# Kernel optimization log

Measured on AMD Instinct MI355X. Metric: run time of the kernel, lower is better.

## Reference

```python
import jax, jax.numpy as jnp
import numpy as np

OBS_LEN, PRED_LEN, N, P = 8, 12, 4096, 32
EH, DH, EMB, BOT, NZ = 64, 128, 64, 1024, 8


def setup_inputs() -> dict:
    key = jax.random.key(0)
    ks = iter(jax.random.split(key, 64))
    rn = lambda shp, s=0.05: (jax.random.normal(next(ks), shp, jnp.float32) * s)
    d = {
        'obs_traj': rn((OBS_LEN, N, 2), 1.0),
        'obs_traj_rel': rn((OBS_LEN, N, 2), 0.5),
        'obs_speed': jax.random.uniform(next(ks), (OBS_LEN, N, 1), jnp.float32),
        'noise': rn((N, NZ), 1.0),
        'enc_emb_W': rn((2, EMB)), 'enc_emb_b': jnp.zeros((EMB,), jnp.float32),
        'enc_Wih': rn((EMB, 4 * EH)), 'enc_Whh': rn((EH, 4 * EH)), 'enc_b': jnp.zeros((4 * EH,), jnp.float32),
        'pool_sp_W': rn((2, 64)), 'pool_sp_b': jnp.zeros((64,), jnp.float32),
        'pool_spd_W': rn((1, 64)), 'pool_spd_b': jnp.zeros((64,), jnp.float32),
        'pool_l1_W': rn((192, 512)), 'pool_l1_b': jnp.zeros((512,), jnp.float32),
        'pool_bn1_g': jnp.ones((512,), jnp.float32), 'pool_bn1_b': jnp.zeros((512,), jnp.float32),
        'pool_l2_W': rn((512, BOT)), 'pool_l2_b': jnp.zeros((BOT,), jnp.float32),
        'pool_bn2_g': jnp.ones((BOT,), jnp.float32), 'pool_bn2_b': jnp.zeros((BOT,), jnp.float32),
        'spd_emb_W': rn((OBS_LEN, 64)), 'spd_emb_b': jnp.zeros((64,), jnp.float32),
        'ctx_l1_W': rn((EH + BOT + 64, 1024)), 'ctx_l1_b': jnp.zeros((1024,), jnp.float32),
        'ctx_bn1_g': jnp.ones((1024,), jnp.float32), 'ctx_bn1_b': jnp.zeros((1024,), jnp.float32),
        'ctx_l2_W': rn((1024, DH - NZ)), 'ctx_l2_b': jnp.zeros((DH - NZ,), jnp.float32),
        'ctx_bn2_g': jnp.ones((DH - NZ,), jnp.float32), 'ctx_bn2_b': jnp.zeros((DH - NZ,), jnp.float32),
        'dec_emb_W': rn((3, EMB)), 'dec_emb_b': jnp.zeros((EMB,), jnp.float32),
        'dec_Wih': rn((EMB, 4 * DH)), 'dec_Whh': rn((DH, 4 * DH)), 'dec_b': jnp.zeros((4 * DH,), jnp.float32),
        'h2p_W': rn((DH, 2)), 'h2p_b': jnp.zeros((2,), jnp.float32),
        'group_size': P,
    }
    return d


def _lstm(xs, Wih, Whh, b, h0, c0):
    # xs: [T, B, in]; PyTorch gate order (i, f, g, o)
    def step(carry, x):
        h, c = carry
        g = x @ Wih + h @ Whh + b
        i, f, gg, o = jnp.split(g, 4, axis=-1)
        c = jax.nn.sigmoid(f) * c + jax.nn.sigmoid(i) * jnp.tanh(gg)
        h = jax.nn.sigmoid(o) * jnp.tanh(c)
        return (h, c), h
    (h, c), _ = jax.lax.scan(step, (h0, c0), xs)
    return h, c


def _bn(x, g, b):
    # BatchNorm1d, eval mode with running_mean=0, running_var=1
    return x * g + b


def reference(obs_traj, obs_traj_rel, obs_speed, noise,
              enc_emb_W, enc_emb_b, enc_Wih, enc_Whh, enc_b,
              pool_sp_W, pool_sp_b, pool_spd_W, pool_spd_b,
              pool_l1_W, pool_l1_b, pool_bn1_g, pool_bn1_b,
              pool_l2_W, pool_l2_b, pool_bn2_g, pool_bn2_b,
              spd_emb_W, spd_emb_b,
              ctx_l1_W, ctx_l1_b, ctx_bn1_g, ctx_bn1_b,
              ctx_l2_W, ctx_l2_b, ctx_bn2_g, ctx_bn2_b,
              dec_emb_W, dec_emb_b, dec_Wih, dec_Whh, dec_b,
              h2p_W, h2p_b, group_size):
    n = obs_traj.shape[1]
    G = n // group_size
    # ---- Encoder: embed rel traj, run LSTM, take final hidden ----
    emb = obs_traj_rel @ enc_emb_W + enc_emb_b                       # [T, N, 64]
    h0 = jnp.zeros((n, EH), emb.dtype)
    final_h, _ = _lstm(emb, enc_Wih, enc_Whh, enc_b, h0, h0)         # [N, 64]
    # ---- PoolHiddenNet (vectorized per-group P x P social pooling) ----
    end_pos = obs_traj[-1].reshape(G, group_size, 2)                 # [G, P, 2]
    end_spd = obs_speed[-1].reshape(G, group_size, 1)                # [G, P, 1]
    hG = final_h.reshape(G, group_size, EH)                          # [G, P, 64]
    # rel[g, i, j] = pos[g, j] - pos[g, i]
    rel = end_pos[:, None, :, :] - end_pos[:, :, None, :]            # [G, P, P, 2]
    rel_e = rel @ pool_sp_W + pool_sp_b                              # [G, P, P, 64]
    spd_e = end_spd @ pool_spd_W + pool_spd_b                        # [G, P, 64]
    Pn = group_size
    feat = jnp.concatenate([
        rel_e,
        jnp.broadcast_to(hG[:, None, :, :], (G, Pn, Pn, EH)),
        jnp.broadcast_to(spd_e[:, None, :, :], (G, Pn, Pn, 64)),
    ], axis=-1)                                                      # [G, P, P, 192]
    h1 = jax.nn.relu(_bn(feat @ pool_l1_W + pool_l1_b, pool_bn1_g, pool_bn1_b))
    h2 = jax.nn.relu(_bn(h1 @ pool_l2_W + pool_l2_b, pool_bn2_g, pool_bn2_b))
    pool_h = jnp.max(h2, axis=2).reshape(n, BOT)                     # max over j -> [N, 1024]
    # ---- speed context: sigmoid(Linear(8 -> 64)) over obs speed history ----
    spd_hist = jnp.transpose(obs_speed[:, :, 0])                     # [N, 8]
    speed_ctx = jax.nn.sigmoid(spd_hist @ spd_emb_W + spd_emb_b)     # [N, 64]
    # ---- mlp_decoder_context + ped-level noise ----
    ctx_in = jnp.concatenate([final_h, pool_h, speed_ctx], axis=1)   # [N, 1152]
    c1 = jax.nn.relu(_bn(ctx_in @ ctx_l1_W + ctx_l1_b, ctx_bn1_g, ctx_bn1_b))
    ctx = jax.nn.relu(_bn(c1 @ ctx_l2_W + ctx_l2_b, ctx_bn2_g, ctx_bn2_b))  # [N, 120]
    dec_h = jnp.concatenate([ctx, noise], axis=1)                    # [N, 128]
    dec_c = jnp.zeros_like(dec_h)
    # ---- Decoder rollout (pred_len steps) ----
    last_pos = obs_traj[-1]
    last_speed = obs_speed[-1]                                       # [N, 1]
    x0 = jnp.concatenate([obs_traj_rel[-1], last_speed], axis=1) @ dec_emb_W + dec_emb_b

    def step(carry, _):
        h, c, x, lp = carry
        g = x @ dec_Wih + h @ dec_Whh + dec_b
        i, f, gg, o = jnp.split(g, 4, axis=-1)
        c = jax.nn.sigmoid(f) * c + jax.nn.sigmoid(i) * jnp.tanh(gg)
        h = jax.nn.sigmoid(o) * jnp.tanh(c)
        rel_pos = h @ h2p_W + h2p_b                                  # [N, 2]
        cur = rel_pos + lp
        x = jnp.concatenate([rel_pos, last_speed], axis=1) @ dec_emb_W + dec_emb_b
        return (h, c, x, cur), rel_pos

    _, rels = jax.lax.scan(step, (dec_h, dec_c, x0, last_pos), None, length=PRED_LEN)
    return rels  # [pred_len, N, 2]
```

## Files before the change

### kernel.cpp

```cpp
#include <hip/hip_runtime.h>

typedef __attribute__((ext_vector_type(8))) short v8s;
typedef __attribute__((ext_vector_type(4))) float v4f;
typedef unsigned short u16;

#define DINL static __device__ __forceinline__

DINL float b2f(u16 u){ union { unsigned uu; float ff; } x; x.uu = ((unsigned)u)<<16; return x.ff; }
DINL u16 f2b(float f){ union { float ff; unsigned uu; } x; x.ff = f; unsigned r = x.uu + 0x7FFFu + ((x.uu>>16)&1u); return (u16)(r>>16); }
DINL u16 f2b_hu(float f){ union { float ff; unsigned uu; } x; x.ff = f; return (u16)((x.uu + 0x8000u)>>16); }
DINL float sigm(float x){ return 1.0f/(1.0f+__expf(-x)); }
DINL float tanh_(float x){ return 2.0f/(1.0f+__expf(-2.0f*x)) - 1.0f; }
DINL float ld(const void* p, int i, int isf){
    return isf ? ((const float*)p)[i] : b2f(((const u16*)p)[i]);
}
DINL void g2lds16(const u16* g, u16* l){
    __builtin_amdgcn_global_load_lds(
        (const __attribute__((address_space(1))) unsigned int*)g,
        (__attribute__((address_space(3))) unsigned int*)l, 16, 0, 0);
}
DINL int detect_isf(const void* obs_speed){
    const u16* p = (const u16*)obs_speed;
    int f = 0;
    for (int i = 0; i < 16; ++i){
        u16 v = p[2*i];
        if ((v & 0x8000u) || v > 0x3F80u) f = 1;
    }
    return f;
}

#define FLAG_OFF 0x000000
#define AUX_OFF  0x000100
#define ENCF_OFF 0x010000
#define DECF_OFF 0x020000
#define CW2T_OFF 0x050000
#define W2T_OFF  0x090000
#define DECH_OFF 0x090000
#define CW1T_OFF 0x190000
#define IT_OFF   0x3D0000
#define IR_OFF   0x3F0000
#define IS_OFF   0x410000
#define INZ_OFF  0x420000
#define IW1H_OFF 0x430000
#define SM_OFF   0x440000
#define CTX_OFF  0x450000
#define AV_OFF   0xD50000
#define BIG_NEED 0x1550000

#define SM_EEW 0
#define SM_EEB 128
#define SM_ENB 192
#define SM_DEW 448
#define SM_DEB 640
#define SM_DNB 704
#define SM_H2W 1216
#define SM_H2B 1472
#define SM_SEW 1536
#define SM_SEB 2048

DINL void trans_tile(const void* in, u16* out, int K, int N, int isf,
                     int bx, int by, int t, float tile[64][65])
{
    const int nbase = bx*64, kbase = by*64;
    const int c = t & 63, r0 = (t >> 6)*16;
    for (int rep = 0; rep < 16; ++rep){
        int r = r0 + rep;
        int n = nbase + c;
        float v = 0.f;
        if (n < N) v = ld(in, (kbase + r)*N + n, isf);
        tile[r][c] = v;
    }
    __syncthreads();
    for (int rep = 0; rep < 16; ++rep){
        int r = r0 + rep;
        out[(size_t)(nbase + r)*K + kbase + c] = f2b(tile[c][r]);
    }
}

__global__ __launch_bounds__(256) void k_prep(
    const void* obs_traj, const void* obs_rel, const void* obs_speed, const void* noise,
    const void* eeW, const void* eeB, const void* enc_Wih, const void* enc_Whh, const void* encB,
    const void* spW, const void* spB, const void* spdW, const void* spdB,
    const void* pool_l1_W, const void* l1B, const void* bn1g, const void* bn1b,
    const void* pool_l2_W, const void* l2b, const void* bn2g, const void* bn2b,
    const void* seW, const void* seB,
    const void* ctx_l1_W, const void* c1b, const void* cbn1g, const void* cbn1b,
    const void* ctx_l2_W, const void* c2b, const void* cbn2g, const void* cbn2b,
    const void* deW, const void* deB, const void* dec_Wih, const void* dec_Whh, const void* decB,
    const void* h2W, const void* h2B,
    int* flag, float* AUX,
    u16* IT, u16* IR, u16* IS, u16* INZ, u16* IW1H, u16* SM,
    u16* W2T, u16* cW1T, u16* cW2T, u16* encF, u16* decF)
{
    __shared__ float tile[64][65];
    __shared__ int sisf;
    const int t = threadIdx.x;
    if (t == 0){
        int f = detect_isf(obs_speed);
        sisf = f;
        if (blockIdx.x == 0) *flag = f;
    }
    __syncthreads();
    const int isf = sisf;
    int bid = blockIdx.x;
    if (bid < 905){
        int idx = bid*256 + t;
        if (idx < 65536){ IT[idx] = f2b(ld(obs_traj, idx, isf)); return; }
        idx -= 65536;
        if (idx < 65536){ IR[idx] = f2b(ld(obs_rel, idx, isf)); return; }
        idx -= 65536;
        if (idx < 32768){ IS[idx] = f2b(ld(obs_speed, idx, isf)); return; }
        idx -= 32768;
        if (idx < 32768){ INZ[idx] = f2b(ld(noise, idx, isf)); return; }
        idx -= 32768;
        if (idx < 32768){ IW1H[idx] = f2b(ld(pool_l1_W, idx + 32768, isf)); return; }
        idx -= 32768;
        if (idx < 128){ SM[SM_EEW + idx] = f2b(ld(eeW, idx, isf)); return; }
        idx -= 128;
        if (idx < 64){ SM[SM_EEB + idx] = f2b(ld(eeB, idx, isf)); return; }
        idx -= 64;
        if (idx < 256){ SM[SM_ENB + idx] = f2b(ld(encB, idx, isf)); return; }
        idx -= 256;
        if (idx < 192){ SM[SM_DEW + idx] = f2b(ld(deW, idx, isf)); return; }
        idx -= 192;
        if (idx < 64){ SM[SM_DEB + idx] = f2b(ld(deB, idx, isf)); return; }
        idx -= 64;
        if (idx < 512){ SM[SM_DNB + idx] = f2b(ld(decB, idx, isf)); return; }
        idx -= 512;
        if (idx < 256){ SM[SM_H2W + idx] = f2b(ld(h2W, idx, isf)); return; }
        idx -= 256;
        if (idx < 2){ SM[SM_H2B + idx] = f2b(ld(h2B, idx, isf)); return; }
        idx -= 2;
        if (idx < 512){ SM[SM_SEW + idx] = f2b(ld(seW, idx, isf)); return; }
        idx -= 512;
        if (idx < 64){ SM[SM_SEB + idx] = f2b(ld(seB, idx, isf)); return; }
        return;
    }
    bid -= 905;
    if (bid < 512){
        int idx = bid*256 + t;
        if (idx < 32768){
            int jj = idx&7, lane = (idx>>3)&63, kcnf = idx>>9;
            int kc = kcnf&3, nf = kcnf>>2;
            int k = kc*32 + (lane>>4)*8 + jj, n = nf*16 + (lane&15);
            encF[idx] = (k < 64) ? f2b(ld(enc_Wih, k*256+n, isf)) : f2b(ld(enc_Whh, (k-64)*256+n, isf));
        } else {
            idx -= 32768;
            int jj = idx&7, lane = (idx>>3)&63, kcnf = idx>>9;
            int kc = kcnf % 6, nf = kcnf / 6;
            int k = kc*32 + (lane>>4)*8 + jj, n = nf*16 + (lane&15);
            decF[idx] = (k < 64) ? f2b(ld(dec_Wih, k*512+n, isf)) : f2b(ld(dec_Whh, (k-64)*512+n, isf));
        }
        return;
    }
    bid -= 512;
    if (bid < 128){ trans_tile(pool_l2_W, W2T, 512, 1024, isf, bid & 15, bid >> 4, t, tile); return; }
    bid -= 128;
    if (bid < 288){ trans_tile(ctx_l1_W, cW1T, 1152, 1024, isf, bid & 15, bid >> 4, t, tile); return; }
    bid -= 288;
    if (bid < 32){ trans_tile(ctx_l2_W, cW2T, 1024, 120, isf, bid & 1, bid >> 1, t, tile); return; }
    bid -= 32;
    {
        int idx = bid*256 + t;
        if (idx < 512){
            int c = idx;
            float m0 = 0.f, m1 = 0.f, qv = 0.f, cv = 0.f;
            for (int e = 0; e < 64; ++e){
                float w1a = ld(pool_l1_W, e*512 + c, isf);
                m0 += ld(spW, e, isf)*w1a;
                m1 += ld(spW, 64+e, isf)*w1a;
                cv += ld(spB, e, isf)*w1a;
                float w1c = ld(pool_l1_W, (128+e)*512 + c, isf);
                qv += ld(spdW, e, isf)*w1c;
                cv += ld(spdB, e, isf)*w1c;
            }
            cv += ld(l1B, c, isf);
            float g1 = ld(bn1g, c, isf), bb1 = ld(bn1b, c, isf);
            AUX[c] = m0; AUX[512+c] = m1; AUX[1024+c] = qv; AUX[1536+c] = cv;
            AUX[2048+c] = g1; AUX[2560+c] = bb1;
            AUX[3072+c] = g1*m0; AUX[3584+c] = g1*m1;
            return;
        }
        idx -= 512;
        if (idx < 1024){
            float g = ld(bn2g, idx, isf);
            AUX[4096+idx] = g; AUX[5120+idx] = ld(l2b, idx, isf)*g + ld(bn2b, idx, isf);
            return;
        }
        idx -= 1024;
        if (idx < 1024){
            float g = ld(cbn1g, idx, isf);
            AUX[6144+idx] = g; AUX[7168+idx] = ld(c1b, idx, isf)*g + ld(cbn1b, idx, isf);
            return;
        }
        idx -= 1024;
        if (idx < 128){
            int c = idx;
            float g  = (c < 120) ? ld(cbn2g, c, isf) : 1.f;
            float bb = (c < 120) ? (ld(c2b, c, isf)*g + ld(cbn2b, c, isf)) : 0.f;
            AUX[8192+c] = g; AUX[8320+c] = bb;
        }
    }
}

__global__ __launch_bounds__(256) void k_encoder(
    const u16* __restrict__ rel, const u16* __restrict__ embW, const u16* __restrict__ embB,
    const u16* __restrict__ encF, const u16* __restrict__ encB,
    const u16* __restrict__ IT, const u16* __restrict__ IS, const u16* __restrict__ IW1H,
    const u16* __restrict__ sW, const u16* __restrict__ sB,
    const float* __restrict__ AUX,
    u16* __restrict__ ctxIn, u16* __restrict__ Avec)
{
    __shared__ __align__(16) u16 Als[16*136];
    __shared__ float pxs[16], pys[16], sps[16];
    const int t = threadIdx.x, pedbase = blockIdx.x*16;
    const int w = t>>6, lane = t&63, quad = lane>>4, l15 = lane&15;
    for (int idx = t; idx < 16*64; idx += 256){ int p = idx>>6, jj = idx&63; Als[p*136 + 64 + jj] = 0; }
    if (t < 16){
        pxs[t] = b2f(IT[7*8192 + (pedbase+t)*2 + 0]);
        pys[t] = b2f(IT[7*8192 + (pedbase+t)*2 + 1]);
        sps[t] = b2f(IS[7*4096 + pedbase + t]);
    }
    {
        int p = t>>4, e0 = (t&15)*4;
        float rx = b2f(rel[(pedbase+p)*2 + 0]);
        float ry = b2f(rel[(pedbase+p)*2 + 1]);
        for (int e = e0; e < e0+4; ++e)
            Als[p*136 + e] = f2b(rx*b2f(embW[e]) + ry*b2f(embW[64+e]) + b2f(embB[e]));
    }
    const int j = w*16 + l15;
    const float bi = b2f(encB[j]), bff = b2f(encB[64+j]), bg = b2f(encB[128+j]), bo = b2f(encB[192+j]);
    float c4[4] = {0.f,0.f,0.f,0.f};
    for (int step = 0; step < 8; ++step){
        __syncthreads();
        v4f acc[4];
        for (int q = 0; q < 4; ++q) acc[q] = (v4f){0.f,0.f,0.f,0.f};
        for (int kc = 0; kc < 4; ++kc){
            v8s a = *(const v8s*)&Als[l15*136 + kc*32 + quad*8];
            for (int q = 0; q < 4; ++q){
                int nf = q*4 + w;
                v8s b = *(const v8s*)&encF[((nf*4 + kc)*64 + lane)*8];
                acc[q] = __builtin_amdgcn_mfma_f32_16x16x32_bf16(a, b, acc[q], 0, 0, 0);
            }
        }
        __syncthreads();
        for (int r = 0; r < 4; ++r){
            float gi = sigm(acc[0][r] + bi), gf = sigm(acc[1][r] + bff);
            float gg = tanh_(acc[2][r] + bg), go = sigm(acc[3][r] + bo);
            c4[r] = gf*c4[r] + gi*gg;
            Als[(quad*4 + r)*136 + 64 + j] = f2b(go*tanh_(c4[r]));
        }
        if (step < 7){
            int p = t>>4, e0 = (t&15)*4;
            float rx = b2f(rel[(step+1)*8192 + (pedbase+p)*2 + 0]);
            float ry = b2f(rel[(step+1)*8192 + (pedbase+p)*2 + 1]);
            for (int e = e0; e < e0+4; ++e)
                Als[p*136 + e] = f2b(rx*b2f(embW[e]) + ry*b2f(embW[64+e]) + b2f(embB[e]));
        }
    }
    __syncthreads();
    for (int idx = t; idx < 1024; idx += 256){
        int p = idx>>6, e = idx&63;
        ctxIn[(size_t)(pedbase+p)*1152 + e] = Als[p*136 + 64 + e];
    }
    {
        const int c0 = (t&127)*4, pg = (t>>7)*8;
        float4 acc[8];
        for (int p = 0; p < 8; ++p) acc[p] = make_float4(0.f,0.f,0.f,0.f);
        for (int e = 0; e < 64; ++e){
            ushort4 wv = *(const ushort4*)(IW1H + e*512 + c0);
            float w0 = b2f(wv.x), w1 = b2f(wv.y), w2 = b2f(wv.z), w3 = b2f(wv.w);
            for (int p = 0; p < 8; ++p){
                float h = b2f(Als[(pg+p)*136 + 64 + e]);
                acc[p].x += h*w0; acc[p].y += h*w1; acc[p].z += h*w2; acc[p].w += h*w3;
            }
        }
        float4 m0 = *(const float4*)(AUX + c0),        m1 = *(const float4*)(AUX + 512 + c0);
        float4 qv = *(const float4*)(AUX + 1024 + c0), cv = *(const float4*)(AUX + 1536 + c0);
        float4 g1 = *(const float4*)(AUX + 2048 + c0), bb = *(const float4*)(AUX + 2560 + c0);
        for (int p = 0; p < 8; ++p){
            float px = pxs[pg+p], py = pys[pg+p], sp = sps[pg+p];
            ushort4 o;
            o.x = f2b(g1.x*(px*m0.x + py*m1.x + sp*qv.x + cv.x + acc[p].x) + bb.x);
            o.y = f2b(g1.y*(px*m0.y + py*m1.y + sp*qv.y + cv.y + acc[p].y) + bb.y);
            o.z = f2b(g1.z*(px*m0.z + py*m1.z + sp*qv.z + cv.z + acc[p].z) + bb.z);
            o.w = f2b(g1.w*(px*m0.w + py*m1.w + sp*qv.w + cv.w + acc[p].w) + bb.w);
            *(ushort4*)&Avec[(size_t)(pedbase+pg+p)*512 + c0] = o;
        }
    }
    {
        int s = t & 63;
        for (int rep = 0; rep < 4; ++rep){
            int p = (t>>6)*4 + rep;
            int nid = pedbase + p;
            float a = b2f(sB[s]);
            for (int tt = 0; tt < 8; ++tt) a += b2f(IS[tt*4096 + nid]) * b2f(sW[tt*64 + s]);
            ctxIn[(size_t)nid*1152 + 1088 + s] = f2b(sigm(a));
        }
    }
}

__global__ __launch_bounds__(256, 3) void k_pool(
    const u16* __restrict__ Avec, const u16* __restrict__ W2T,
    const u16* __restrict__ IT, const float* __restrict__ AUX,
    u16* __restrict__ ctxIn)
{
    __shared__ __align__(16) u16 Als[64*72];
    __shared__ __align__(16) u16 Bls[256*64];
    __shared__ float auxM[1024];
    __shared__ float pxs[2], pys[2];
    const int t = threadIdx.x;
    const int g = blockIdx.x >> 4, ip = blockIdx.x & 15;
    const int n0 = blockIdx.y * 256;
    const int w = t>>6, lane = t&63, quad = lane>>4, l15 = lane&15;
    const int aj = t>>3, ao = t&7;
    for (int i = t; i < 1024; i += 256) auxM[i] = AUX[3072 + i];
    if (t < 2){
        pxs[t] = b2f(IT[7*8192 + (g*32 + ip*2 + t)*2 + 0]);
        pys[t] = b2f(IT[7*8192 + (g*32 + ip*2 + t)*2 + 1]);
    }
    const u16* bsrc = W2T + (size_t)(n0 + w*8 + (lane>>3))*512 + (size_t)(((lane&7) ^ (lane>>3)))*8;
    u16* bdst = &Bls[w*512];
    const u16* arow = Avec + (size_t)(g*32+aj)*512 + ao*8;
    v4f acc[4][4];
    for (int mf = 0; mf < 4; ++mf) for (int nf = 0; nf < 4; ++nf) acc[mf][nf] = (v4f){0.f,0.f,0.f,0.f};
    union { v8s v; u16 u[8]; } av;
    av.v = *(const v8s*)arow;
    for (int ch = 0; ch < 8; ++ch){
        const int k0 = ch*64;
        __syncthreads();
        for (int it = 0; it < 8; ++it)
            g2lds16(bsrc + k0 + it*16384, bdst + it*2048);
        {
            float a0[8], m0a[8], m1a[8];
            for (int i = 0; i < 8; ++i) a0[i] = b2f(av.u[i]);
            *(float4*)(m0a)   = *(const float4*)&auxM[k0 + ao*8];
            *(float4*)(m0a+4) = *(const float4*)&auxM[k0 + ao*8 + 4];
            *(float4*)(m1a)   = *(const float4*)&auxM[512 + k0 + ao*8];
            *(float4*)(m1a+4) = *(const float4*)&auxM[512 + k0 + ao*8 + 4];
            for (int il = 0; il < 2; ++il){
                float npx = -pxs[il], npy = -pys[il];
                union { v8s v; u16 u[8]; } pk;
                for (int i = 0; i < 8; ++i){
                    float v = __builtin_fmaf(npy, m1a[i], __builtin_fmaf(npx, m0a[i], a0[i]));
                    pk.u[i] = f2b_hu(fmaxf(v, 0.f));
                }
                *(v8s*)&Als[(il*32+aj)*72 + ao*8] = pk.v;
            }
        }
        if (ch < 7) av.v = *(const v8s*)(arow + (ch+1)*64);
        __syncthreads();
        for (int kc = 0; kc < 2; ++kc){
            v8s af[4];
            for (int mf = 0; mf < 4; ++mf)
                af[mf] = *(const v8s*)&Als[(mf*16 + l15)*72 + kc*32 + quad*8];
            const int sl = ((kc*4 + quad) ^ (l15&7))*8;
            #pragma unroll
            for (int nf = 0; nf < 4; ++nf){
                v8s bf = *(const v8s*)&Bls[(w*64 + nf*16 + l15)*64 + sl];
                acc[0][nf] = __builtin_amdgcn_mfma_f32_16x16x32_bf16(af[0], bf, acc[0][nf], 0, 0, 0);
                acc[1][nf] = __builtin_amdgcn_mfma_f32_16x16x32_bf16(af[1], bf, acc[1][nf], 0, 0, 0);
                acc[2][nf] = __builtin_amdgcn_mfma_f32_16x16x32_bf16(af[2], bf, acc[2][nf], 0, 0, 0);
                acc[3][nf] = __builtin_amdgcn_mfma_f32_16x16x32_bf16(af[3], bf, acc[3][nf], 0, 0, 0);
            }
        }
    }
    const float* S2 = AUX + 4096; const float* B2 = AUX + 5120;
    for (int nf = 0; nf < 4; ++nf){
        int n = n0 + w*64 + nf*16 + l15;
        float s = S2[n], bb = B2[n];
        float mm0 = 0.f, mm1 = 0.f;
        for (int mf = 0; mf < 2; ++mf) for (int r = 0; r < 4; ++r) mm0 = fmaxf(mm0, fmaxf(s*acc[mf][nf][r] + bb, 0.f));
        for (int mf = 2; mf < 4; ++mf) for (int r = 0; r < 4; ++r) mm1 = fmaxf(mm1, fmaxf(s*acc[mf][nf][r] + bb, 0.f));
        mm0 = fmaxf(mm0, __shfl_xor(mm0, 16)); mm0 = fmaxf(mm0, __shfl_xor(mm0, 32));
        mm1 = fmaxf(mm1, __shfl_xor(mm1, 16)); mm1 = fmaxf(mm1, __shfl_xor(mm1, 32));
        if (quad == 0) ctxIn[(size_t)(g*32 + ip*2 + 0)*1152 + 64 + n] = f2b(mm0);
        if (quad == 1) ctxIn[(size_t)(g*32 + ip*2 + 1)*1152 + 64 + n] = f2b(mm1);
    }
}

template<int MF>
__global__ __launch_bounds__(256) void k_gemm_bt(
    const u16* __restrict__ A, int lda, const u16* __restrict__ BT,
    const float* __restrict__ S, const float* __restrict__ Bb,
    u16* __restrict__ out, int ldo, int K, int validN,
    const u16* __restrict__ noisep)
{
    __shared__ __align__(16) u16 Als[MF*32*72];
    __shared__ __align__(16) u16 Bls[128*72];
    const int t = threadIdx.x;
    const int m0 = blockIdx.x*(MF*32), n0 = blockIdx.y*128;
    const int w = t>>6, lane = t&63, quad = lane>>4, l15 = lane&15;
    const int rw = w>>1, cw = w&1;
    v4f acc[MF][4];
    for (int mf = 0; mf < MF; ++mf) for (int nf = 0; nf < 4; ++nf) acc[mf][nf] = (v4f){0.f,0.f,0.f,0.f};
    const int nch = K >> 6;
    for (int ch = 0; ch < nch; ++ch){
        const int k0 = ch*64;
        __syncthreads();
        if (MF == 4){
            const int srow = t>>1, sh = t&1;
            const u16* srcA = A + (size_t)(m0+srow)*lda + k0 + sh*32;
            u16* dstA = &Als[srow*72 + sh*32];
            ((v8s*)dstA)[0] = ((const v8s*)srcA)[0];
            ((v8s*)dstA)[1] = ((const v8s*)srcA)[1];
            ((v8s*)dstA)[2] = ((const v8s*)srcA)[2];
            ((v8s*)dstA)[3] = ((const v8s*)srcA)[3];
        } else {
            const int srow = t>>2, sh = t&3;
            const u16* srcA = A + (size_t)(m0+srow)*lda + k0 + sh*16;
            u16* dstA = &Als[srow*72 + sh*16];
            ((v8s*)dstA)[0] = ((const v8s*)srcA)[0];
            ((v8s*)dstA)[1] = ((const v8s*)srcA)[1];
        }
        {
            const int srow = t>>1, sh = t&1;
            const u16* srcB = BT + (size_t)(n0+srow)*K + k0 + sh*32;
            u16* dstB = &Bls[srow*72 + sh*32];
            ((v8s*)dstB)[0] = ((const v8s*)srcB)[0];
            ((v8s*)dstB)[1] = ((const v8s*)srcB)[1];
            ((v8s*)dstB)[2] = ((const v8s*)srcB)[2];
            ((v8s*)dstB)[3] = ((const v8s*)srcB)[3];
        }
        __syncthreads();
        for (int kc = 0; kc < 2; ++kc){
            v8s af[MF], bf[4];
            for (int mf = 0; mf < MF; ++mf) af[mf] = *(const v8s*)&Als[(rw*(MF*16) + mf*16 + l15)*72 + kc*32 + quad*8];
            for (int nf = 0; nf < 4; ++nf) bf[nf] = *(const v8s*)&Bls[(cw*64 + nf*16 + l15)*72 + kc*32 + quad*8];
            for (int mf = 0; mf < MF; ++mf)
                for (int nf = 0; nf < 4; ++nf)
                    acc[mf][nf] = __builtin_amdgcn_mfma_f32_16x16x32_bf16(af[mf], bf[nf], acc[mf][nf], 0, 0, 0);
        }
    }
    for (int nf = 0; nf < 4; ++nf){
        int n = n0 + cw*64 + nf*16 + l15;
        bool okn = (n < validN);
        float s = okn ? S[n] : 0.f, bb = okn ? Bb[n] : 0.f;
        bool okz = (!okn) && (noisep != nullptr) && (n < 128);
        for (int mf = 0; mf < MF; ++mf){
            int m = m0 + rw*(MF*16) + mf*16 + quad*4;
            for (int r = 0; r < 4; ++r){
                float v = fmaxf(s*acc[mf][nf][r] + bb, 0.f);
                if (okn) out[(size_t)(m+r)*ldo + n] = f2b(v);
                else if (okz) out[(size_t)(m+r)*ldo + n] = noisep[(size_t)(m+r)*8 + (n - 120)];
            }
        }
    }
}

__global__ __launch_bounds__(256) void k_decoder(
    const u16* __restrict__ decH0, const u16* __restrict__ decF, const u16* __restrict__ decB,
    const u16* __restrict__ dembW, const u16* __restrict__ dembB,
    const u16* __restrict__ h2pW, const u16* __restrict__ h2pB,
    const u16* __restrict__ obs_rel, const u16* __restrict__ obs_speed,
    const int* __restrict__ flag, void* __restrict__ outp)
{
    __shared__ __align__(16) u16 Als[16*200];
    __shared__ float rps[16][2];
    __shared__ float sps[16];
    __shared__ float h2ps[256];
    const int t = threadIdx.x, pedbase = blockIdx.x*16;
    const int w = t>>6, lane = t&63, quad = lane>>4, l15 = lane&15;
    const int isf = *flag;
    for (int idx = t; idx < 2048; idx += 256){
        int p = idx>>7, jj = idx&127;
        Als[p*200 + 64 + jj] = decH0[(pedbase+p)*128 + jj];
    }
    h2ps[t] = b2f(h2pW[t]);
    if (t < 16) sps[t] = b2f(obs_speed[7*4096 + pedbase + t]);
    if (t < 32){ int p = t>>1, cmp = t&1; rps[p][cmp] = b2f(obs_rel[7*8192 + (pedbase+p)*2 + cmp]); }
    __syncthreads();
    {
        int p = t>>4, e0 = (t&15)*4;
        for (int e = e0; e < e0+4; ++e){
            float v = rps[p][0]*b2f(dembW[e]) + rps[p][1]*b2f(dembW[64+e]) + sps[p]*b2f(dembW[128+e]) + b2f(dembB[e]);
            Als[p*200 + e] = f2b(v);
        }
    }
    float bI[2], bF[2], bG[2], bO[2];
    for (int nfl = 0; nfl < 2; ++nfl){
        int j = w*32 + nfl*16 + l15;
        bI[nfl] = b2f(decB[j]); bF[nfl] = b2f(decB[128+j]);
        bG[nfl] = b2f(decB[256+j]); bO[nfl] = b2f(decB[384+j]);
    }
    float c8[2][4] = {{0.f,0.f,0.f,0.f},{0.f,0.f,0.f,0.f}};
    for (int s = 0; s < 12; ++s){
        __syncthreads();
        v4f acc[4][2];
        for (int q = 0; q < 4; ++q) for (int nfl = 0; nfl < 2; ++nfl) acc[q][nfl] = (v4f){0.f,0.f,0.f,0.f};
        for (int kc = 0; kc < 6; ++kc){
            v8s a = *(const v8s*)&Als[l15*200 + kc*32 + quad*8];
            for (int q = 0; q < 4; ++q){
                for (int nfl = 0; nfl < 2; ++nfl){
                    int nf = q*8 + w*2 + nfl;
                    v8s b = *(const v8s*)&decF[((nf*6 + kc)*64 + lane)*8];
                    acc[q][nfl] = __builtin_amdgcn_mfma_f32_16x16x32_bf16(a, b, acc[q][nfl], 0, 0, 0);
                }
            }
        }
        __syncthreads();
        for (int nfl = 0; nfl < 2; ++nfl){
            int j = w*32 + nfl*16 + l15;
            for (int r = 0; r < 4; ++r){
                float gi = sigm(acc[0][nfl][r] + bI[nfl]), gf = sigm(acc[1][nfl][r] + bF[nfl]);
                float gg = tanh_(acc[2][nfl][r] + bG[nfl]), go = sigm(acc[3][nfl][r] + bO[nfl]);
                c8[nfl][r] = gf*c8[nfl][r] + gi*gg;
                Als[(quad*4 + r)*200 + 64 + j] = f2b(go*tanh_(c8[nfl][r]));
            }
        }
        __syncthreads();
        {
            int p = t>>4, cmp = (t>>3)&1, part = t&7;
            float rp = 0.f;
            int j0 = part*16;
            for (int jj = j0; jj < j0+16; ++jj)
                rp += b2f(Als[p*200 + 64 + jj]) * h2ps[jj*2 + cmp];
            rp += __shfl_xor(rp, 1);
            rp += __shfl_xor(rp, 2);
            rp += __shfl_xor(rp, 4);
            if (part == 0){
                rp += b2f(h2pB[cmp]);
                int oi = s*8192 + (pedbase+p)*2 + cmp;
                if (isf) ((float*)outp)[oi] = rp;
                else     ((u16*)outp)[oi]   = f2b(rp);
                rps[p][cmp] = rp;
            }
        }
        __syncthreads();
        {
            int p = t>>4, e0 = (t&15)*4;
            for (int e = e0; e < e0+4; ++e){
                float v = rps[p][0]*b2f(dembW[e]) + rps[p][1]*b2f(dembW[64+e]) + sps[p]*b2f(dembW[128+e]) + b2f(dembB[e]);
                Als[p*200 + e] = f2b(v);
            }
        }
    }
}

extern "C" void kernel_launch(void* const* d_in, const int* in_sizes, int n_in,
                              void* d_out, int out_size, void* d_ws, size_t ws_size,
                              hipStream_t stream)
{
    (void)in_sizes; (void)n_in; (void)out_size;
    const void* obs_traj  = d_in[0];
    const void* obs_rel   = d_in[1];
    const void* obs_speed = d_in[2];
    const void* noise     = d_in[3];
    const void* enc_emb_W = d_in[4];
    const void* enc_emb_b = d_in[5];
    const void* enc_Wih   = d_in[6];
    const void* enc_Whh   = d_in[7];
    const void* enc_b     = d_in[8];
    const void* pool_sp_W = d_in[9];
    const void* pool_sp_b = d_in[10];
    const void* pool_spd_W= d_in[11];
    const void* pool_spd_b= d_in[12];
    const void* pool_l1_W = d_in[13];
    const void* pool_l1_b = d_in[14];
    const void* pool_bn1_g= d_in[15];
    const void* pool_bn1_b= d_in[16];
    const void* pool_l2_W = d_in[17];
    const void* pool_l2_b = d_in[18];
    const void* pool_bn2_g= d_in[19];
    const void* pool_bn2_b= d_in[20];
    const void* spd_emb_W = d_in[21];
    const void* spd_emb_b = d_in[22];
    const void* ctx_l1_W  = d_in[23];
    const void* ctx_l1_b  = d_in[24];
    const void* ctx_bn1_g = d_in[25];
    const void* ctx_bn1_b = d_in[26];
    const void* ctx_l2_W  = d_in[27];
    const void* ctx_l2_b  = d_in[28];
    const void* ctx_bn2_g = d_in[29];
    const void* ctx_bn2_b = d_in[30];
    const void* dec_emb_W = d_in[31];
    const void* dec_emb_b = d_in[32];
    const void* dec_Wih   = d_in[33];
    const void* dec_Whh   = d_in[34];
    const void* dec_b     = d_in[35];
    const void* h2p_W     = d_in[36];
    const void* h2p_b     = d_in[37];

    char* ws = (char*)d_ws;
    int*   flag  = (int*)  (ws + FLAG_OFF);
    float* AUX   = (float*)(ws + AUX_OFF);
    u16*   encF  = (u16*)  (ws + ENCF_OFF);
    u16*   decF  = (u16*)  (ws + DECF_OFF);
    u16*   cW2T  = (u16*)  (ws + CW2T_OFF);
    u16*   W2T   = (u16*)  (ws + W2T_OFF);
    u16*   decH  = (u16*)  (ws + DECH_OFF);
    u16*   cW1T  = (u16*)  (ws + CW1T_OFF);
    u16*   IT    = (u16*)  (ws + IT_OFF);
    u16*   IR    = (u16*)  (ws + IR_OFF);
    u16*   IS    = (u16*)  (ws + IS_OFF);
    u16*   INZ   = (u16*)  (ws + INZ_OFF);
    u16*   IW1H  = (u16*)  (ws + IW1H_OFF);
    u16*   SM    = (u16*)  (ws + SM_OFF);
    u16*   ctxIn = (u16*)  (ws + CTX_OFF);
    u16*   Avec  = (u16*)  (ws + AV_OFF);
    u16*   c1    = (u16*)  (ws + AV_OFF);
    const bool big = (ws_size >= (size_t)BIG_NEED);

    k_prep<<<dim3(1876), dim3(256), 0, stream>>>(
        obs_traj, obs_rel, obs_speed, noise,
        enc_emb_W, enc_emb_b, enc_Wih, enc_Whh, enc_b,
        pool_sp_W, pool_sp_b, pool_spd_W, pool_spd_b,
        pool_l1_W, pool_l1_b, pool_bn1_g, pool_bn1_b,
        pool_l2_W, pool_l2_b, pool_bn2_g, pool_bn2_b,
        spd_emb_W, spd_emb_b,
        ctx_l1_W, ctx_l1_b, ctx_bn1_g, ctx_bn1_b,
        ctx_l2_W, ctx_l2_b, ctx_bn2_g, ctx_bn2_b,
        dec_emb_W, dec_emb_b, dec_Wih, dec_Whh, dec_b,
        h2p_W, h2p_b,
        flag, AUX, IT, IR, IS, INZ, IW1H, SM,
        W2T, cW1T, cW2T, encF, decF);
    k_encoder<<<dim3(256), dim3(256), 0, stream>>>(
        IR, SM + SM_EEW, SM + SM_EEB, encF, SM + SM_ENB,
        IT, IS, IW1H, SM + SM_SEW, SM + SM_SEB, AUX, ctxIn, Avec);
    k_pool<<<dim3(2048, 4), dim3(256), 0, stream>>>(Avec, W2T, IT, AUX, ctxIn);
    if (big){
        k_gemm_bt<4><<<dim3(32, 8), dim3(256), 0, stream>>>(
            ctxIn, 1152, cW1T, AUX + 6144, AUX + 7168, c1, 1024, 1152, 1024, (const u16*)nullptr);
        k_gemm_bt<2><<<dim3(64, 1), dim3(256), 0, stream>>>(
            c1, 1024, cW2T, AUX + 8192, AUX + 8320, decH, 128, 1024, 120, INZ);
    } else {
        k_gemm_bt<4><<<dim3(16, 8), dim3(256), 0, stream>>>(
            ctxIn, 1152, cW1T, AUX + 6144, AUX + 7168, c1, 1024, 1152, 1024, (const u16*)nullptr);
        k_gemm_bt<2><<<dim3(32, 1), dim3(256), 0, stream>>>(
            c1, 1024, cW2T, AUX + 8192, AUX + 8320, decH, 128, 1024, 120, INZ);
        k_gemm_bt<4><<<dim3(16, 8), dim3(256), 0, stream>>>(
            ctxIn + (size_t)2048*1152, 1152, cW1T, AUX + 6144, AUX + 7168, c1, 1024, 1152, 1024, (const u16*)nullptr);
        k_gemm_bt<2><<<dim3(32, 1), dim3(256), 0, stream>>>(
            c1, 1024, cW2T, AUX + 8192, AUX + 8320, decH + (size_t)2048*128, 128, 1024, 120, INZ + (size_t)2048*8);
    }
    k_decoder<<<dim3(256), dim3(256), 0, stream>>>(
        decH, decF, SM + SM_DNB, SM + SM_DEW, SM + SM_DEB,
        SM + SM_H2W, SM + SM_H2B, IR, IS, flag, d_out);
}
```

Baseline: 439.2 us.

## Build the pool hidden layer once per block and loop over all output tiles

The pooling kernel now computes the full 64x512 first-layer activation (relative-position term plus ReLU) once into LDS with an XOR swizzle. It then loops over eight 128-column tiles of the second-layer weights inside a single block, instead of launching four y-blocks that each recompute the activation. This removes redundant activation recomputation and Avec reads, and cuts the grid from 8192 to 2048 blocks. In exchange LDS use grows to about 80KB per block, occupancy is lowered to 2 blocks, and each block runs a longer serial loop with two barriers per chunk.

Result: slower. 454.5 us (+3.5%).

```diff
diff --git a/kernel.cpp b/kernel.cpp
--- a/kernel.cpp
+++ b/kernel.cpp
@@ -300,82 +300,96 @@
     }
 }
 
-__global__ __launch_bounds__(256, 3) void k_pool(
+__global__ __launch_bounds__(256, 2) void k_pool(
     const u16* __restrict__ Avec, const u16* __restrict__ W2T,
     const u16* __restrict__ IT, const float* __restrict__ AUX,
     u16* __restrict__ ctxIn)
 {
-    __shared__ __align__(16) u16 Als[64*72];
-    __shared__ __align__(16) u16 Bls[256*64];
-    __shared__ float auxM[1024];
-    __shared__ float pxs[2], pys[2];
+    __shared__ __align__(16) u16 H1[64*512];
+    __shared__ __align__(16) u16 Bls[128*64];
     const int t = threadIdx.x;
     const int g = blockIdx.x >> 4, ip = blockIdx.x & 15;
-    const int n0 = blockIdx.y * 256;
     const int w = t>>6, lane = t&63, quad = lane>>4, l15 = lane&15;
     const int aj = t>>3, ao = t&7;
-    for (int i = t; i < 1024; i += 256) auxM[i] = AUX[3072 + i];
-    if (t < 2){
-        pxs[t] = b2f(IT[7*8192 + (g*32 + ip*2 + t)*2 + 0]);
-        pys[t] = b2f(IT[7*8192 + (g*32 + ip*2 + t)*2 + 1]);
-    }
-    const u16* bsrc = W2T + (size_t)(n0 + w*8 + (lane>>3))*512 + (size_t)(((lane&7) ^ (lane>>3)))*8;
+    const float px0 = b2f(IT[7*8192 + (g*32 + ip*2 + 0)*2 + 0]);
+    const float py0 = b2f(IT[7*8192 + (g*32 + ip*2 + 0)*2 + 1]);
+    const float px1 = b2f(IT[7*8192 + (g*32 + ip*2 + 1)*2 + 0]);
+    const float py1 = b2f(IT[7*8192 + (g*32 + ip*2 + 1)*2 + 1]);
+    const float* M0G = AUX + 3072;
+    const float* M1G = AUX + 3584;
+    const u16* arow = Avec + (size_t)(g*32 + aj)*512 + ao*8;
+    #pragma unroll
+    for (int ch = 0; ch < 8; ++ch){
+        union { v8s v; u16 u[8]; } av;
+        av.v = *(const v8s*)(arow + ch*64);
+        float a0[8], m0a[8], m1a[8];
+        *(float4*)(m0a)   = *(const float4*)&M0G[ch*64 + ao*8];
+        *(float4*)(m0a+4) = *(const float4*)&M0G[ch*64 + ao*8 + 4];
+        *(float4*)(m1a)   = *(const float4*)&M1G[ch*64 + ao*8];
+        *(float4*)(m1a+4) = *(const float4*)&M1G[ch*64 + ao*8 + 4];
+        for (int i = 0; i < 8; ++i) a0[i] = b2f(av.u[i]);
+        #pragma unroll
+        for (int il = 0; il < 2; ++il){
+            const float npx = (il == 0) ? -px0 : -px1;
+            const float npy = (il == 0) ? -py0 : -py1;
+            int r = il*32 + aj;
+            int slot = (ch*8 + ao) ^ (r & 7);
+            union { v8s v; u16 u[8]; } pk;
+            for (int i = 0; i < 8; ++i){
+                float v = __builtin_fmaf(npy, m1a[i], __builtin_fmaf(npx, m0a[i], a0[i]));
+                pk.u[i] = f2b_hu(fmaxf(v, 0.f));
+            }
+            *(v8s*)&H1[r*512 + slot*8] = pk.v;
+        }
+    }
+    const u16* bsrc = W2T + (size_t)(w*8 + (lane>>3))*512 + (size_t)((lane&7) ^ (lane>>3))*8;
     u16* bdst = &Bls[w*512];
-    const u16* arow = Avec + (size_t)(g*32+aj)*512 + ao*8;
-    v4f acc[4][4];
-    for (int mf = 0; mf < 4; ++mf) for (int nf = 0; nf < 4; ++nf) acc[mf][nf] = (v4f){0.f,0.f,0.f,0.f};
-    union { v8s v; u16 u[8]; } av;
-    av.v = *(const v8s*)arow;
-    for (int ch = 0; ch < 8; ++ch){
-        const int k0 = ch*64;
-        __syncthreads();
-        for (int it = 0; it < 8; ++it)
-            g2lds16(bsrc + k0 + it*16384, bdst + it*2048);
-        {
-            float a0[8], m0a[8], m1a[8];
-            for (int i = 0; i < 8; ++i) a0[i] = b2f(av.u[i]);
-            *(float4*)(m0a)   = *(const float4*)&auxM[k0 + ao*8];
-            *(float4*)(m0a+4) = *(const float4*)&auxM[k0 + ao*8 + 4];
-            *(float4*)(m1a)   = *(const float4*)&auxM[512 + k0 + ao*8];
-            *(float4*)(m1a+4) = *(const float4*)&auxM[512 + k0 + ao*8 + 4];
-            for (int il = 0; il < 2; ++il){
-                float npx = -pxs[il], npy = -pys[il];
-                union { v8s v; u16 u[8]; } pk;
-                for (int i = 0; i < 8; ++i){
-                    float v = __builtin_fmaf(npy, m1a[i], __builtin_fmaf(npx, m0a[i], a0[i]));
-                    pk.u[i] = f2b_hu(fmaxf(v, 0.f));
+    const float* S2 = AUX + 4096;
+    const float* B2 = AUX + 5120;
+    __syncthreads();
+    for (int ntile = 0; ntile < 8; ++ntile){
+        v4f acc[4][2];
+        for (int mf = 0; mf < 4; ++mf) for (int nf = 0; nf < 2; ++nf) acc[mf][nf] = (v4f){0.f,0.f,0.f,0.f};
+        const u16* bsn = bsrc + (size_t)ntile*128*512;
+        for (int ch = 0; ch < 8; ++ch){
+            __syncthreads();
+            #pragma unroll
+            for (int it = 0; it < 4; ++it)
+                g2lds16(bsn + it*16384 + ch*64, bdst + it*2048);
+            __syncthreads();
+            #pragma unroll
+            for (int kc = 0; kc < 2; ++kc){
+                const int cgl = kc*4 + quad;
+                v8s af[4];
+                #pragma unroll
+                for (int mf = 0; mf < 4; ++mf){
+                    int r = mf*16 + l15;
+                    int slot = ch*8 + (cgl ^ (l15 & 7));
+                    af[mf] = *(const v8s*)&H1[r*512 + slot*8];
                 }
-                *(v8s*)&Als[(il*32+aj)*72 + ao*8] = pk.v;
-            }
-        }
-        if (ch < 7) av.v = *(const v8s*)(arow + (ch+1)*64);
-        __syncthreads();
-        for (int kc = 0; kc < 2; ++kc){
-            v8s af[4];
-            for (int mf = 0; mf < 4; ++mf)
-                af[mf] = *(const v8s*)&Als[(mf*16 + l15)*72 + kc*32 + quad*8];
-            const int sl = ((kc*4 + quad) ^ (l15&7))*8;
-            #pragma unroll
-            for (int nf = 0; nf < 4; ++nf){
-                v8s bf = *(const v8s*)&Bls[(w*64 + nf*16 + l15)*64 + sl];
-                acc[0][nf] = __builtin_amdgcn_mfma_f32_16x16x32_bf16(af[0], bf, acc[0][nf], 0, 0, 0);
-                acc[1][nf] = __builtin_amdgcn_mfma_f32_16x16x32_bf16(af[1], bf, acc[1][nf], 0, 0, 0);
-                acc[2][nf] = __builtin_amdgcn_mfma_f32_16x16x32_bf16(af[2], bf, acc[2][nf], 0, 0, 0);
-                acc[3][nf] = __builtin_amdgcn_mfma_f32_16x16x32_bf16(af[3], bf, acc[3][nf], 0, 0, 0);
-            }
-        }
-    }
-    const float* S2 = AUX + 4096; const float* B2 = AUX + 5120;
-    for (int nf = 0; nf < 4; ++nf){
-        int n = n0 + w*64 + nf*16 + l15;
-        float s = S2[n], bb = B2[n];
-        float mm0 = 0.f, mm1 = 0.f;
-        for (int mf = 0; mf < 2; ++mf) for (int r = 0; r < 4; ++r) mm0 = fmaxf(mm0, fmaxf(s*acc[mf][nf][r] + bb, 0.f));
-        for (int mf = 2; mf < 4; ++mf) for (int r = 0; r < 4; ++r) mm1 = fmaxf(mm1, fmaxf(s*acc[mf][nf][r] + bb, 0.f));
-        mm0 = fmaxf(mm0, __shfl_xor(mm0, 16)); mm0 = fmaxf(mm0, __shfl_xor(mm0, 32));
-        mm1 = fmaxf(mm1, __shfl_xor(mm1, 16)); mm1 = fmaxf(mm1, __shfl_xor(mm1, 32));
-        if (quad == 0) ctxIn[(size_t)(g*32 + ip*2 + 0)*1152 + 64 + n] = f2b(mm0);
-        if (quad == 1) ctxIn[(size_t)(g*32 + ip*2 + 1)*1152 + 64 + n] = f2b(mm1);
+                const int bslot = cgl ^ (l15 & 7);
+                #pragma unroll
+                for (int nf = 0; nf < 2; ++nf){
+                    int col = w*32 + nf*16 + l15;
+                    v8s bf = *(const v8s*)&Bls[col*64 + bslot*8];
+                    acc[0][nf] = __builtin_amdgcn_mfma_f32_16x16x32_bf16(af[0], bf, acc[0][nf], 0, 0, 0);
+                    acc[1][nf] = __builtin_amdgcn_mfma_f32_16x16x32_bf16(af[1], bf, acc[1][nf], 0, 0, 0);
+                    acc[2][nf] = __builtin_amdgcn_mfma_f32_16x16x32_bf16(af[2], bf, acc[2][nf], 0, 0, 0);
+                    acc[3][nf] = __builtin_amdgcn_mfma_f32_16x16x32_bf16(af[3], bf, acc[3][nf], 0, 0, 0);
+                }
+            }
+        }
+        for (int nf = 0; nf < 2; ++nf){
+            int n = ntile*128 + w*32 + nf*16 + l15;
+            float s = S2[n], bb = B2[n];
+            float mm0 = 0.f, mm1 = 0.f;
+            for (int mf = 0; mf < 2; ++mf) for (int r = 0; r < 4; ++r) mm0 = fmaxf(mm0, fmaxf(s*acc[mf][nf][r] + bb, 0.f));
+            for (int mf = 2; mf < 4; ++mf) for (int r = 0; r < 4; ++r) mm1 = fmaxf(mm1, fmaxf(s*acc[mf][nf][r] + bb, 0.f));
+            mm0 = fmaxf(mm0, __shfl_xor(mm0, 16)); mm0 = fmaxf(mm0, __shfl_xor(mm0, 32));
+            mm1 = fmaxf(mm1, __shfl_xor(mm1, 16)); mm1 = fmaxf(mm1, __shfl_xor(mm1, 32));
+            if (quad == 0) ctxIn[(size_t)(g*32 + ip*2 + 0)*1152 + 64 + n] = f2b(mm0);
+            if (quad == 1) ctxIn[(size_t)(g*32 + ip*2 + 1)*1152 + 64 + n] = f2b(mm1);
+        }
     }
 }
 
@@ -617,7 +631,7 @@
     k_encoder<<<dim3(256), dim3(256), 0, stream>>>(
         IR, SM + SM_EEW, SM + SM_EEB, encF, SM + SM_ENB,
         IT, IS, IW1H, SM + SM_SEW, SM + SM_SEB, AUX, ctxIn, Avec);
-    k_pool<<<dim3(2048, 4), dim3(256), 0, stream>>>(Avec, W2T, IT, AUX, ctxIn);
+    k_pool<<<dim3(2048), dim3(256), 0, stream>>>(Avec, W2T, IT, AUX, ctxIn);
     if (big){
         k_gemm_bt<4><<<dim3(32, 8), dim3(256), 0, stream>>>(
             ctxIn, 1152, cW1T, AUX + 6144, AUX + 7168, c1, 1024, 1152, 1024, (const u16*)nullptr);
```
